# Kernel tuning notes

Hardware: AMD Instinct MI355X
Metric: run time of the kernel (lower is better)

## Reference

```python
import jax, jax.numpy as jnp
from jax import lax
import numpy as np

B, N, D = 64, 512, 2


def _dtw_cost(x, y):
    """Exact DTW with L1 point distance. x: (n, d), y: (m, d).
    Returns terminal cumulative cost D[n-1, m-1], which equals the sum of
    ||x_i - y_j||_1 over the optimal warping path (what the torch module
    accumulates after fastdtw path search)."""
    # pairwise L1 cost matrix (n, m)
    C = jnp.sum(jnp.abs(x[:, None, :] - y[None, :, :]), axis=-1)
    row0 = jnp.cumsum(C[0])  # D[0, :]
    big = jnp.asarray(jnp.inf, C.dtype)

    def row_step(prev, c):
        # prev = D[i-1, :]; c = C[i, :]
        diag = jnp.concatenate([jnp.full((1,), big), prev[:-1]])  # D[i-1, j-1]

        def col_step(left, inp):
            ci, up, dg = inp
            cur = ci + jnp.minimum(jnp.minimum(up, dg), left)
            return cur, cur

        _, cur = lax.scan(col_step, big, (c, prev, diag))
        return cur, None

    final_row, _ = lax.scan(row_step, row0, C[1:])
    return final_row[-1]


def setup_inputs() -> dict:
    key = jax.random.key(0)
    k1, k2 = jax.random.split(key)
    pred = jax.random.normal(k1, (B, N, D), dtype=jnp.float32)
    target = jax.random.normal(k2, (B, N, D), dtype=jnp.float32)
    return {"pred": pred, "target": target}


def reference(pred, target):
    # mean over batch of per-sequence DTW path L1 loss
    per_batch = jax.vmap(_dtw_cost)(pred, target)  # (B,)
    return jnp.mean(per_batch)
```

## Files before the change

kernel.cpp:

```cpp
#include <hip/hip_runtime.h>
#include <math.h>


constexpr int NSEQ  = 512;
constexpr int BATCH = 64;
constexpr int P     = 8;
constexpr int LANES = 64;

__device__ __forceinline__ float dpp_wshr1_inf(float v) {
    int r = __builtin_amdgcn_update_dpp(0x7F800000, __float_as_int(v),
                                        0x138, 0xF, 0xF, false);
    return __int_as_float(r);
}

__global__ __launch_bounds__(LANES) void dtw_strip(
    const float* __restrict__ pred,
    const float* __restrict__ target,
    float* __restrict__ per_batch)
{
    const int b = blockIdx.x;
    const int j = threadIdx.x;

    __shared__ float2 xs[NSEQ + 2];

    #pragma unroll
    for (int t = 0; t < NSEQ / LANES; ++t) {
        const int idx = t * LANES + j;
        xs[idx] = reinterpret_cast<const float2*>(pred)[b * NSEQ + idx];
    }
    float Y0[P], Y1[P];
    #pragma unroll
    for (int c = 0; c < P; ++c) {
        const float2 y = reinterpret_cast<const float2*>(target)[b * NSEQ + j * P + c];
        Y0[c] = y.x; Y1[c] = y.y;
    }
    __syncthreads();

    const float INF = __builtin_inff();
    float prev[P];
    #pragma unroll
    for (int c = 0; c < P; ++c) prev[c] = INF;
    float dg0 = INF;

    auto STEP = [&](float left, float2 x) {
        float pm1 = prev[0];
        float v = fabsf(x.x - Y0[0]) + fabsf(x.y - Y1[0])
                + fminf(fminf(pm1, dg0), left);
        prev[0] = v;
        #pragma unroll
        for (int c = 1; c < P; ++c) {
            const float pc = prev[c];
            v = fabsf(x.x - Y0[c]) + fabsf(x.y - Y1[c])
              + fminf(fminf(pc, pm1), v);
            prev[c] = v;
            pm1 = pc;
        }
    };

    if (j == 0) STEP(0.0f, xs[0]);

    float2 xc;
    {
        const int i1 = 1 - j;
        xc = xs[i1 > 0 ? i1 : 0];
    }

    for (int k = 1; k < LANES; ++k) {
        const float left = dpp_wshr1_inf(prev[P - 1]);
        const int ip = k + 1 - j;
        const float2 xn = xs[ip > 0 ? ip : 0];
        if (k - j >= 0) STEP(left, xc);
        dg0 = left;
        xc = xn;
    }

    #pragma unroll 4
    for (int k = LANES; k < NSEQ; ++k) {
        const float left = dpp_wshr1_inf(prev[P - 1]);
        const float2 xn = xs[k + 1 - j];
        STEP(left, xc);
        dg0 = left;
        xc = xn;
    }

    for (int k = NSEQ; k < NSEQ + LANES - 1; ++k) {
        const float left = dpp_wshr1_inf(prev[P - 1]);
        const int ip = k + 1 - j;
        const float2 xn = xs[ip < NSEQ ? ip : NSEQ - 1];
        if (k - j < NSEQ) STEP(left, xc);
        dg0 = left;
        xc = xn;
    }

    if (j == LANES - 1) per_batch[b] = prev[P - 1];
}

__global__ void dtw_reduce(const float* __restrict__ per_batch,
                           float* __restrict__ out)
{
    float v = per_batch[threadIdx.x];
    #pragma unroll
    for (int off = 32; off >= 1; off >>= 1)
        v += __shfl_down(v, off);
    if (threadIdx.x == 0)
        out[0] = v * (1.0f / BATCH);
}

extern "C" void kernel_launch(void* const* d_in, const int* in_sizes, int n_in,
                              void* d_out, int out_size, void* d_ws, size_t ws_size,
                              hipStream_t stream) {
    const float* pred   = (const float*)d_in[0];
    const float* target = (const float*)d_in[1];
    float* out = (float*)d_out;
    float* per_batch = (float*)d_ws;

    dtw_strip<<<BATCH, LANES, 0, stream>>>(pred, target, per_batch);
    dtw_reduce<<<1, 64, 0, stream>>>(per_batch, out);
}
```

Measured before the change: 56.56 us.

## Fuse DTW reduction via last-block atomic and block-unroll wavefront steps

Merges the separate reduction kernel into the DTW kernel using a global atomic counter, so the last block to finish does the batch mean. The counter is zeroed with a memset before launch. The wavefront loop is restructured into blocks of four steps with x values prefetched from a padded shared array, which removes the clamped index math. Boundary steps use select-based predication instead of branches, and negated targets in packed vector form allow packed adds. The memset is an extra stream operation, and the atomic plus threadfence add a little work at the end of every block.

```diff
diff --git a/kernel.cpp b/kernel.cpp
--- a/kernel.cpp
+++ b/kernel.cpp
@@ -1,11 +1,15 @@
 #include <hip/hip_runtime.h>
 #include <math.h>
 
+
+typedef float f32x2 __attribute__((ext_vector_type(2)));
 
 constexpr int NSEQ  = 512;
 constexpr int BATCH = 64;
 constexpr int P     = 8;
 constexpr int LANES = 64;
+constexpr int FRONT = 64;
+constexpr int XSN   = FRONT + 581;
 
 __device__ __forceinline__ float dpp_wshr1_inf(float v) {
     int r = __builtin_amdgcn_update_dpp(0x7F800000, __float_as_int(v),
@@ -13,26 +17,27 @@
     return __int_as_float(r);
 }
 
-__global__ __launch_bounds__(LANES) void dtw_strip(
+__global__ __launch_bounds__(LANES) void dtw_fused(
     const float* __restrict__ pred,
     const float* __restrict__ target,
-    float* __restrict__ per_batch)
+    float* __restrict__ out,
+    float* __restrict__ ws)
 {
     const int b = blockIdx.x;
     const int j = threadIdx.x;
 
-    __shared__ float2 xs[NSEQ + 2];
+    __shared__ f32x2 xs[XSN];
 
     #pragma unroll
     for (int t = 0; t < NSEQ / LANES; ++t) {
         const int idx = t * LANES + j;
-        xs[idx] = reinterpret_cast<const float2*>(pred)[b * NSEQ + idx];
+        xs[FRONT + idx] = reinterpret_cast<const f32x2*>(pred)[b * NSEQ + idx];
     }
-    float Y0[P], Y1[P];
+    f32x2 nY[P];
     #pragma unroll
     for (int c = 0; c < P; ++c) {
-        const float2 y = reinterpret_cast<const float2*>(target)[b * NSEQ + j * P + c];
-        Y0[c] = y.x; Y1[c] = y.y;
+        const f32x2 y = reinterpret_cast<const f32x2*>(target)[b * NSEQ + j * P + c];
+        nY[c].x = -y.x; nY[c].y = -y.y;
     }
     __syncthreads();
 
@@ -42,68 +47,83 @@
     for (int c = 0; c < P; ++c) prev[c] = INF;
     float dg0 = INF;
 
-    auto STEP = [&](float left, float2 x) {
-        float pm1 = prev[0];
-        float v = fabsf(x.x - Y0[0]) + fabsf(x.y - Y1[0])
-                + fminf(fminf(pm1, dg0), left);
+    if (j == 0) {
+        const f32x2 x = xs[FRONT];
+        f32x2 d0 = x + nY[0];
+        float v = fabsf(d0.x) + fabsf(d0.y);
         prev[0] = v;
         #pragma unroll
         for (int c = 1; c < P; ++c) {
+            f32x2 dc = x + nY[c];
+            v += fabsf(dc.x) + fabsf(dc.y);
+            prev[c] = v;
+        }
+    }
+
+    auto step = [&](float left, f32x2 x, int kk, bool guard) {
+        float v_[P];
+        {
+            f32x2 d = x + nY[0];
+            v_[0] = fabsf(d.x) + fabsf(d.y) + fminf(fminf(prev[0], dg0), left);
+        }
+        float pm1 = prev[0];
+        #pragma unroll
+        for (int c = 1; c < P; ++c) {
+            f32x2 d = x + nY[c];
             const float pc = prev[c];
-            v = fabsf(x.x - Y0[c]) + fabsf(x.y - Y1[c])
-              + fminf(fminf(pc, pm1), v);
-            prev[c] = v;
+            v_[c] = fabsf(d.x) + fabsf(d.y) + fminf(fminf(pc, pm1), v_[c - 1]);
             pm1 = pc;
         }
+        if (guard) {
+            const bool act = (unsigned)(kk - j) < (unsigned)NSEQ;
+            #pragma unroll
+            for (int c = 0; c < P; ++c) prev[c] = act ? v_[c] : prev[c];
+        } else {
+            #pragma unroll
+            for (int c = 0; c < P; ++c) prev[c] = v_[c];
+        }
+        dg0 = left;
     };
 
-    if (j == 0) STEP(0.0f, xs[0]);
-
-    float2 xc;
+    f32x2 r0, r1, r2, r3;
     {
-        const int i1 = 1 - j;
-        xc = xs[i1 > 0 ? i1 : 0];
+        const int base = FRONT + 1 - j;
+        r0 = xs[base]; r1 = xs[base + 1]; r2 = xs[base + 2]; r3 = xs[base + 3];
     }
 
-    for (int k = 1; k < LANES; ++k) {
-        const float left = dpp_wshr1_inf(prev[P - 1]);
-        const int ip = k + 1 - j;
-        const float2 xn = xs[ip > 0 ? ip : 0];
-        if (k - j >= 0) STEP(left, xc);
-        dg0 = left;
-        xc = xn;
+    auto block4 = [&](int k4, bool guard) {
+        const int base = FRONT + k4 + 4 - j;
+        const f32x2 n0 = xs[base],     n1 = xs[base + 1];
+        const f32x2 n2 = xs[base + 2], n3 = xs[base + 3];
+        float left;
+        left = dpp_wshr1_inf(prev[P - 1]); step(left, r0, k4 + 0, guard);
+        left = dpp_wshr1_inf(prev[P - 1]); step(left, r1, k4 + 1, guard);
+        left = dpp_wshr1_inf(prev[P - 1]); step(left, r2, k4 + 2, guard);
+        left = dpp_wshr1_inf(prev[P - 1]); step(left, r3, k4 + 3, guard);
+        r0 = n0; r1 = n1; r2 = n2; r3 = n3;
+    };
+
+    #pragma unroll 1
+    for (int k4 = 1; k4 <= 61; k4 += 4)   block4(k4, true);
+    #pragma unroll 1
+    for (int k4 = 65; k4 <= 505; k4 += 4) block4(k4, false);
+    #pragma unroll 1
+    for (int k4 = 509; k4 <= 573; k4 += 4) block4(k4, true);
+
+    float* per_batch = ws;
+    unsigned* flag = reinterpret_cast<unsigned*>(ws + BATCH);
+    if (j == LANES - 1) per_batch[b] = prev[P - 1];
+    __threadfence();
+    unsigned old = 0;
+    if (j == 0) old = atomicAdd(flag, 1u);
+    old = __shfl(old, 0);
+    if (old == BATCH - 1) {
+        __threadfence();
+        float v = per_batch[j];
+        #pragma unroll
+        for (int off = 32; off >= 1; off >>= 1) v += __shfl_down(v, off);
+        if (j == 0) out[0] = v * (1.0f / BATCH);
     }
-
-    #pragma unroll 4
-    for (int k = LANES; k < NSEQ; ++k) {
-        const float left = dpp_wshr1_inf(prev[P - 1]);
-        const float2 xn = xs[k + 1 - j];
-        STEP(left, xc);
-        dg0 = left;
-        xc = xn;
-    }
-
-    for (int k = NSEQ; k < NSEQ + LANES - 1; ++k) {
-        const float left = dpp_wshr1_inf(prev[P - 1]);
-        const int ip = k + 1 - j;
-        const float2 xn = xs[ip < NSEQ ? ip : NSEQ - 1];
-        if (k - j < NSEQ) STEP(left, xc);
-        dg0 = left;
-        xc = xn;
-    }
-
-    if (j == LANES - 1) per_batch[b] = prev[P - 1];
-}
-
-__global__ void dtw_reduce(const float* __restrict__ per_batch,
-                           float* __restrict__ out)
-{
-    float v = per_batch[threadIdx.x];
-    #pragma unroll
-    for (int off = 32; off >= 1; off >>= 1)
-        v += __shfl_down(v, off);
-    if (threadIdx.x == 0)
-        out[0] = v * (1.0f / BATCH);
 }
 
 extern "C" void kernel_launch(void* const* d_in, const int* in_sizes, int n_in,
@@ -112,8 +132,8 @@
     const float* pred   = (const float*)d_in[0];
     const float* target = (const float*)d_in[1];
     float* out = (float*)d_out;
-    float* per_batch = (float*)d_ws;
+    float* ws  = (float*)d_ws;
 
-    dtw_strip<<<BATCH, LANES, 0, stream>>>(pred, target, per_batch);
-    dtw_reduce<<<1, 64, 0, stream>>>(per_batch, out);
+    hipMemsetAsync((char*)d_ws + BATCH * sizeof(float), 0, sizeof(unsigned), stream);
+    dtw_fused<<<BATCH, LANES, 0, stream>>>(pred, target, out, ws);
 }
```

After: 58.23 us. 2.9% more time.
